# Kernel tuning notes

Hardware: AMD Instinct MI355X
Metric: run time of the kernel (lower is better)

## Reference

```python
import jax, jax.numpy as jnp
import numpy as np

B, N, C = 128, 2048, 3
VL, PN = 256, 128  # vector_length, prediction_num
NEG_SLOPE = 0.01   # torch LeakyReLU default
BN_EPS = 1e-5


def _lin(key, fin, fout):
    k1, k2 = jax.random.split(key)
    lim = 1.0 / np.sqrt(fin)
    W = jax.random.uniform(k1, (fin, fout), minval=-lim, maxval=lim, dtype=jnp.float32)
    b = jax.random.uniform(k2, (fout,), minval=-lim, maxval=lim, dtype=jnp.float32)
    return W, b


def setup_inputs() -> dict:
    key = jax.random.key(0)
    ks = jax.random.split(key, 14)
    x = jax.random.normal(ks[0], (B, N, C), dtype=jnp.float32)
    lengths = jnp.maximum(jax.random.randint(ks[1], (B,), 0, N), 1).astype(jnp.int32)
    eps = jax.random.normal(ks[2], (B, VL), dtype=jnp.float32)
    W1, b1 = _lin(ks[3], C, 64)
    W2, b2 = _lin(ks[4], 64, 64)
    W3, b3 = _lin(ks[5], 64, 128)
    W4, b4 = _lin(ks[6], 128, 1024)
    Wf, bf = _lin(ks[7], 1024, 1024)
    Wmu, bmu = _lin(ks[8], 1024, VL)
    Wlv, blv = _lin(ks[9], 1024, VL)
    Wd1, bd1 = _lin(ks[10], VL, 1024)
    Wd2, bd2 = _lin(ks[11], 1024, 1024)
    Wd3, bd3 = _lin(ks[12], 1024, PN * C)
    g1 = jnp.ones((1024,), jnp.float32); be1 = jnp.zeros((1024,), jnp.float32)
    g2 = jnp.ones((1024,), jnp.float32); be2 = jnp.zeros((1024,), jnp.float32)
    return dict(x=x, lengths=lengths, eps=eps,
                W1=W1, b1=b1, W2=W2, b2=b2, W3=W3, b3=b3, W4=W4, b4=b4,
                Wf=Wf, bf=bf, Wmu=Wmu, bmu=bmu, Wlv=Wlv, blv=blv,
                Wd1=Wd1, bd1=bd1, g1=g1, be1=be1,
                Wd2=Wd2, bd2=bd2, g2=g2, be2=be2,
                Wd3=Wd3, bd3=bd3)


def _lrelu(h):
    return jnp.where(h > 0, h, NEG_SLOPE * h)


def _bn(h, g, b):
    # BatchNorm1d in training mode: biased batch stats
    m = h.mean(axis=0)
    v = h.var(axis=0)
    return (h - m) * jax.lax.rsqrt(v + BN_EPS) * g + b


def reference(x, lengths, eps,
              W1, b1, W2, b2, W3, b3, W4, b4,
              Wf, bf, Wmu, bmu, Wlv, blv,
              Wd1, bd1, g1, be1, Wd2, bd2, g2, be2, Wd3, bd3):
    # --- pointnet per-point MLP (batched over padded [B,N,C]) ---
    h = _lrelu(x @ W1 + b1)          # [B,N,64]
    h = _lrelu(h @ W2 + b2)          # [B,N,64]
    h = _lrelu(h @ W3 + b3)          # [B,N,128]
    h = _lrelu(h @ W4 + b4)          # [B,N,1024]
    # masked max over points (ragged -> padded+mask)
    mask = jnp.arange(N)[None, :] < lengths[:, None]   # [B,N]
    h = jnp.where(mask[:, :, None], h, -jnp.inf)
    pooled = jnp.max(h, axis=1)      # [B,1024]
    # --- encoder head ---
    e = _lrelu(pooled @ Wf + bf)
    mu = e @ Wmu + bmu               # [B,VL]
    logvar = e @ Wlv + blv           # [B,VL]
    # --- reparameterize ---
    z = mu + eps * jnp.exp(0.5 * logvar)
    # --- decoder: Linear+BN+LeakyReLU x2, final Linear ---
    d = _lrelu(_bn(z @ Wd1 + bd1, g1, be1))
    d = _lrelu(_bn(d @ Wd2 + bd2, g2, be2))
    y = (d @ Wd3 + bd3).reshape(-1, PN, C)   # [B,PN,C]
    return (y, mu, logvar)
```

## Files before the change

kernel.cpp:

```cpp
#include <hip/hip_runtime.h>
#include <hip/hip_bf16.h>
#include <math.h>

#define NEG_SLOPE 0.01f

typedef short short8 __attribute__((ext_vector_type(8)));
typedef float f32x4 __attribute__((ext_vector_type(4)));

__device__ __forceinline__ float lrelu(float v) { return v > 0.0f ? v : NEG_SLOPE * v; }

__device__ __forceinline__ short f2bf(float f) {
    __hip_bfloat16 h = __float2bfloat16(f);
    return __builtin_bit_cast(short, h);
}
__device__ __forceinline__ float bf2f(short s) {
    __hip_bfloat16 h = __builtin_bit_cast(__hip_bfloat16, s);
    return __bfloat162float(h);
}

__global__ __launch_bounds__(256) void pack_all(
    const float* __restrict__ W4, const float* __restrict__ Wf,
    const float* __restrict__ Wmu, const float* __restrict__ Wlv,
    const float* __restrict__ Wd1, const float* __restrict__ Wd2,
    const float* __restrict__ Wd3, const float* __restrict__ W2,
    const float* __restrict__ W3,
    short* __restrict__ F4, short* __restrict__ Ff, short* __restrict__ Fmuvl,
    short* __restrict__ Fd1, short* __restrict__ Fd2, short* __restrict__ Fd3,
    short* __restrict__ F2, short* __restrict__ F3)
{
    int bid = blockIdx.x;
    const float* src = nullptr; short* dst = nullptr; int K = 0, N = 0; int muvl = 0;
    if      (bid < 64)   { src = W4;  dst = F4;    K = 128;  N = 1024; }
    else if (bid < 576)  { src = Wf;  dst = Ff;    K = 1024; N = 1024; bid -= 64; }
    else if (bid < 832)  { src = nullptr; dst = Fmuvl; K = 1024; N = 512; muvl = 1; bid -= 576; }
    else if (bid < 960)  { src = Wd1; dst = Fd1;   K = 256;  N = 1024; bid -= 832; }
    else if (bid < 1472) { src = Wd2; dst = Fd2;   K = 1024; N = 1024; bid -= 960; }
    else if (bid < 1664) { src = Wd3; dst = Fd3;   K = 1024; N = 384;  bid -= 1472; }
    else if (bid < 1666) { src = W2;  dst = F2;    K = 64;   N = 64;   bid -= 1664; }
    else                 { src = W3;  dst = F3;    K = 64;   N = 128;  bid -= 1666; }

    const int fragid = bid * 4 + (threadIdx.x >> 6);
    const int lane   = threadIdx.x & 63;
    const int K32    = K >> 5;
    const int t   = fragid / (K32 * 4);
    const int rem = fragid - t * K32 * 4;
    const int ks  = rem >> 2;
    const int n   = rem & 3;
    const int col   = t * 64 + n * 16 + (lane & 15);
    const int kbase = ks * 32 + (lane >> 4) * 8;

    short8 v;
#pragma unroll
    for (int e = 0; e < 8; ++e) {
        float f;
        if (muvl) f = (col < 256) ? Wmu[(size_t)(kbase + e) * 256 + col]
                                  : Wlv[(size_t)(kbase + e) * 256 + col - 256];
        else      f = src[(size_t)(kbase + e) * N + col];
        v[e] = f2bf(f);
    }
    *(short8*)&dst[(size_t)fragid * 512 + lane * 8] = v;
}

#define LOADPAIR(BUF, T, P)                                                   \
    _Pragma("unroll")                                                         \
    for (int kk = 0; kk < 2; ++kk)                                            \
        _Pragma("unroll")                                                     \
        for (int n = 0; n < 4; ++n)                                           \
            BUF[kk * 4 + n] = *(const short8*)&F4[                            \
                (size_t)(((((T) * 4 + (P) * 2 + kk) * 4) + n) * 64 + lane) * 8];

#define MFMAPAIR(BUF, KS0)                                                    \
    _Pragma("unroll")                                                         \
    for (int kk = 0; kk < 2; ++kk)                                            \
        _Pragma("unroll")                                                     \
        for (int n = 0; n < 4; ++n)                                           \
            _Pragma("unroll")                                                 \
            for (int m = 0; m < 4; ++m)                                       \
                acc[m][n] = __builtin_amdgcn_mfma_f32_16x16x32_bf16(          \
                    af[m][(KS0) + kk], BUF[kk * 4 + n], acc[m][n], 0, 0, 0);

__global__ __launch_bounds__(128, 2) void fused_pointnet_kernel(
    const float* __restrict__ x, const int* __restrict__ lengths,
    const float* __restrict__ W1, const float* __restrict__ b1,
    const float* __restrict__ b2, const float* __restrict__ b3,
    const short* __restrict__ F2, const short* __restrict__ F3,
    const short* __restrict__ F4,
    short* __restrict__ partials)
{
    const int tid   = threadIdx.x;
    const int b     = blockIdx.x & 127;
    const int chunk = blockIdx.x >> 7;
    const int len   = lengths[b];
    if (chunk * 128 >= len) return;

    __shared__ short At[128 * 128];
    const int lane = tid & 63;
    const int w    = tid >> 6;
    short* Aw = At + w * 8192;
    const int gid  = b * 2048 + chunk * 128 + tid;

    {
        const float x0 = x[gid * 3 + 0];
        const float x1 = x[gid * 3 + 1];
        const float x2 = x[gid * 3 + 2];
#pragma unroll
        for (int q = 0; q < 8; ++q) {
            short8 pv;
#pragma unroll
            for (int e = 0; e < 8; ++e) {
                int c = q * 8 + e;
                float v = b1[c];
                v = fmaf(x0, W1[c], v);
                v = fmaf(x1, W1[64 + c], v);
                v = fmaf(x2, W1[128 + c], v);
                pv[e] = f2bf(lrelu(v));
            }
            *(short8*)&Aw[lane * 64 + ((q ^ (lane & 7)) * 8)] = pv;
        }
    }

    {
        short8 a2[4][2];
#pragma unroll
        for (int m = 0; m < 4; ++m)
#pragma unroll
            for (int ks = 0; ks < 2; ++ks) {
                int rl = m * 16 + (lane & 15);
                int kch = ks * 4 + (lane >> 4);
                a2[m][ks] = *(const short8*)&Aw[rl * 64 + ((kch ^ (rl & 7)) * 8)];
            }
        short8 b2f[2][4];
#pragma unroll
        for (int ks = 0; ks < 2; ++ks)
#pragma unroll
            for (int n = 0; n < 4; ++n)
                b2f[ks][n] = *(const short8*)&F2[(size_t)(ks * 4 + n) * 512 + lane * 8];

        f32x4 acc2[4][4];
#pragma unroll
        for (int m = 0; m < 4; ++m)
#pragma unroll
            for (int n = 0; n < 4; ++n) acc2[m][n] = 0;
#pragma unroll
        for (int ks = 0; ks < 2; ++ks)
#pragma unroll
            for (int n = 0; n < 4; ++n)
#pragma unroll
                for (int m = 0; m < 4; ++m)
                    acc2[m][n] = __builtin_amdgcn_mfma_f32_16x16x32_bf16(
                        a2[m][ks], b2f[ks][n], acc2[m][n], 0, 0, 0);

#pragma unroll
        for (int n = 0; n < 4; ++n) {
            int col = n * 16 + (lane & 15);
            float bv = b2[col];
            int colch = col >> 3;
#pragma unroll
            for (int m = 0; m < 4; ++m)
#pragma unroll
                for (int r = 0; r < 4; ++r) {
                    int rl = m * 16 + (lane >> 4) * 4 + r;
                    Aw[4096 + rl * 64 + ((colch ^ (rl & 7)) * 8) + (col & 7)] =
                        f2bf(lrelu(acc2[m][n][r] + bv));
                }
        }
    }

    short8 a3[4][2];
#pragma unroll
    for (int m = 0; m < 4; ++m)
#pragma unroll
        for (int ks = 0; ks < 2; ++ks) {
            int rl = m * 16 + (lane & 15);
            int kch = ks * 4 + (lane >> 4);
            a3[m][ks] = *(const short8*)&Aw[4096 + rl * 64 + ((kch ^ (rl & 7)) * 8)];
        }
#pragma unroll
    for (int half = 0; half < 2; ++half) {
        short8 b3f[2][4];
#pragma unroll
        for (int ks = 0; ks < 2; ++ks)
#pragma unroll
            for (int n = 0; n < 4; ++n)
                b3f[ks][n] = *(const short8*)&F3[(size_t)(half * 8 + ks * 4 + n) * 512 + lane * 8];

        f32x4 acc3[4][4];
#pragma unroll
        for (int m = 0; m < 4; ++m)
#pragma unroll
            for (int n = 0; n < 4; ++n) acc3[m][n] = 0;
#pragma unroll
        for (int ks = 0; ks < 2; ++ks)
#pragma unroll
            for (int n = 0; n < 4; ++n)
#pragma unroll
                for (int m = 0; m < 4; ++m)
                    acc3[m][n] = __builtin_amdgcn_mfma_f32_16x16x32_bf16(
                        a3[m][ks], b3f[ks][n], acc3[m][n], 0, 0, 0);

#pragma unroll
        for (int n = 0; n < 4; ++n) {
            int col = half * 64 + n * 16 + (lane & 15);
            float bv = b3[col];
            int colch = col >> 3;
#pragma unroll
            for (int m = 0; m < 4; ++m)
#pragma unroll
                for (int r = 0; r < 4; ++r) {
                    int rl = m * 16 + (lane >> 4) * 4 + r;
                    Aw[rl * 128 + ((colch ^ (rl & 7)) * 8) + (col & 7)] =
                        f2bf(lrelu(acc3[m][n][r] + bv));
                }
        }
    }

    short8 af[4][4];
#pragma unroll
    for (int m = 0; m < 4; ++m)
#pragma unroll
        for (int ks = 0; ks < 4; ++ks) {
            int rl = m * 16 + (lane & 15);
            int ch = (ks * 4 + (lane >> 4)) ^ (rl & 7);
            af[m][ks] = *(const short8*)&Aw[rl * 128 + ch * 8];
        }

    const size_t pb = ((size_t)(b * 16 + chunk) * 2 + w) * 1024;

    short8 bufA[8], bufB[8];
    LOADPAIR(bufA, 0, 0);
    for (int t = 0; t < 16; ++t) {
        f32x4 acc[4][4];
#pragma unroll
        for (int m = 0; m < 4; ++m)
#pragma unroll
            for (int n = 0; n < 4; ++n) acc[m][n] = 0;

        LOADPAIR(bufB, t, 1);
        MFMAPAIR(bufA, 0);
        if (t < 15) LOADPAIR(bufA, t + 1, 0);
        MFMAPAIR(bufB, 2);

#pragma unroll
        for (int n = 0; n < 4; ++n) {
            float v = -INFINITY;
#pragma unroll
            for (int m = 0; m < 4; ++m)
#pragma unroll
                for (int r = 0; r < 4; ++r) {
                    int rloc = w * 64 + m * 16 + (lane >> 4) * 4 + r;
                    bool valid = (chunk * 128 + rloc) < len;
                    v = fmaxf(v, valid ? acc[m][n][r] : -INFINITY);
                }
            v = fmaxf(v, __shfl_xor(v, 16));
            v = fmaxf(v, __shfl_xor(v, 32));
            if (lane < 16) partials[pb + t * 64 + n * 16 + lane] = f2bf(v);
        }
    }
}

__global__ __launch_bounds__(256) void reduce_pool_kernel(
    const short* __restrict__ partials, const int* __restrict__ lengths,
    const float* __restrict__ b4, short* __restrict__ pooled)
{
    const int b = blockIdx.x;
    const int nlive = (lengths[b] + 127) >> 7;
    for (int i = threadIdx.x; i < 1024; i += 256) {
        float m = -INFINITY;
        for (int j = 0; j < nlive; ++j) {
            m = fmaxf(m, bf2f(partials[((size_t)(b * 16 + j) * 2 + 0) * 1024 + i]));
            m = fmaxf(m, bf2f(partials[((size_t)(b * 16 + j) * 2 + 1) * 1024 + i]));
        }
        pooled[(size_t)b * 1024 + i] = f2bf(lrelu(m + b4[i]));
    }
}

template<int MF>
__global__ __launch_bounds__(256) void gemm_tail(
    const short* __restrict__ A, const short* __restrict__ Wfrag,
    const float* __restrict__ bias,
    const float* __restrict__ g, const float* __restrict__ be,
    float* __restrict__ outF, short* __restrict__ outB,
    int K, int Nout, int flags)
{
    __shared__ float bns[4][32];
    __shared__ float bnq[4][32];

    const int tid = threadIdx.x, lane = tid & 63, w = tid >> 6;
    const int K32 = K >> 5;
    const int c0  = blockIdx.x * 32;
    const int tt  = blockIdx.x >> 1;
    const int hf  = blockIdx.x & 1;
    const int row0  = (MF == 2) ? 0 : blockIdx.y * 64;
    const int arow0 = row0 + w * (MF * 16) + (lane & 15);
    const int koff  = (lane >> 4) * 8;

    f32x4 acc[MF][2];
#pragma unroll
    for (int m = 0; m < MF; ++m) { acc[m][0] = 0; acc[m][1] = 0; }

    short8 aC[MF], bC[2], aN[MF], bN[2];
#pragma unroll
    for (int m = 0; m < MF; ++m)
        aC[m] = *(const short8*)&A[(size_t)(arow0 + m * 16) * K + koff];
#pragma unroll
    for (int n = 0; n < 2; ++n)
        bC[n] = *(const short8*)&Wfrag[(size_t)((tt * K32) * 4 + hf * 2 + n) * 512 + lane * 8];

    for (int ks = 0; ks < K32; ks += 2) {
#pragma unroll
        for (int m = 0; m < MF; ++m)
            aN[m] = *(const short8*)&A[(size_t)(arow0 + m * 16) * K + (ks + 1) * 32 + koff];
#pragma unroll
        for (int n = 0; n < 2; ++n)
            bN[n] = *(const short8*)&Wfrag[(size_t)((tt * K32 + ks + 1) * 4 + hf * 2 + n) * 512 + lane * 8];
#pragma unroll
        for (int n = 0; n < 2; ++n)
#pragma unroll
            for (int m = 0; m < MF; ++m)
                acc[m][n] = __builtin_amdgcn_mfma_f32_16x16x32_bf16(aC[m], bC[n], acc[m][n], 0, 0, 0);
        if (ks + 2 < K32) {
#pragma unroll
            for (int m = 0; m < MF; ++m)
                aC[m] = *(const short8*)&A[(size_t)(arow0 + m * 16) * K + (ks + 2) * 32 + koff];
#pragma unroll
            for (int n = 0; n < 2; ++n)
                bC[n] = *(const short8*)&Wfrag[(size_t)((tt * K32 + ks + 2) * 4 + hf * 2 + n) * 512 + lane * 8];
        }
#pragma unroll
        for (int n = 0; n < 2; ++n)
#pragma unroll
            for (int m = 0; m < MF; ++m)
                acc[m][n] = __builtin_amdgcn_mfma_f32_16x16x32_bf16(aN[m], bN[n], acc[m][n], 0, 0, 0);
    }

    if ((flags & 2) && MF == 2) {
#pragma unroll
        for (int n = 0; n < 2; ++n) {
            float s = 0.f, q = 0.f;
#pragma unroll
            for (int m = 0; m < MF; ++m)
#pragma unroll
                for (int r = 0; r < 4; ++r) {
                    float v = acc[m][n][r];
                    s += v; q = fmaf(v, v, q);
                }
            s += __shfl_xor(s, 16); s += __shfl_xor(s, 32);
            q += __shfl_xor(q, 16); q += __shfl_xor(q, 32);
            if (lane < 16) { bns[w][n * 16 + lane] = s; bnq[w][n * 16 + lane] = q; }
        }
        __syncthreads();
#pragma unroll
        for (int n = 0; n < 2; ++n) {
            int cl = n * 16 + (lane & 15);
            float s = bns[0][cl] + bns[1][cl] + bns[2][cl] + bns[3][cl];
            float q = bnq[0][cl] + bnq[1][cl] + bnq[2][cl] + bnq[3][cl];
            float mean = s * (1.0f / 128.0f);
            float var  = q * (1.0f / 128.0f) - mean * mean;
            float rs   = 1.0f / sqrtf(var + 1e-5f);
            float gg   = g[c0 + cl] * rs;
            float bb   = be[c0 + cl] - mean * gg;
#pragma unroll
            for (int m = 0; m < MF; ++m)
#pragma unroll
                for (int r = 0; r < 4; ++r)
                    acc[m][n][r] = fmaf(acc[m][n][r], gg, bb);
        }
    } else if (bias) {
#pragma unroll
        for (int n = 0; n < 2; ++n) {
            float bv = bias[c0 + n * 16 + (lane & 15)];
#pragma unroll
            for (int m = 0; m < MF; ++m)
#pragma unroll
                for (int r = 0; r < 4; ++r) acc[m][n][r] += bv;
        }
    }

    if (flags & 1) {
#pragma unroll
        for (int m = 0; m < MF; ++m)
#pragma unroll
            for (int n = 0; n < 2; ++n)
#pragma unroll
                for (int r = 0; r < 4; ++r) acc[m][n][r] = lrelu(acc[m][n][r]);
    }

#pragma unroll
    for (int m = 0; m < MF; ++m)
#pragma unroll
        for (int n = 0; n < 2; ++n)
#pragma unroll
            for (int r = 0; r < 4; ++r) {
                int row = row0 + w * (MF * 16) + m * 16 + (lane >> 4) * 4 + r;
                int col = c0 + n * 16 + (lane & 15);
                if (flags & 4) outB[(size_t)row * Nout + col] = f2bf(acc[m][n][r]);
                else           outF[(size_t)row * Nout + col] = acc[m][n][r];
            }
}

__global__ __launch_bounds__(256) void gemm_muvlz(
    const short* __restrict__ A, const short* __restrict__ Fmuvl,
    const float* __restrict__ bmu, const float* __restrict__ blv,
    const float* __restrict__ eps,
    float* __restrict__ mu_out, float* __restrict__ lv_out,
    short* __restrict__ zbuf)
{
    const int tid = threadIdx.x, lane = tid & 63, w = tid >> 6;
    const int c0 = blockIdx.x * 32;
    const int tt = blockIdx.x >> 1;
    const int hf = blockIdx.x & 1;
    const int row0 = blockIdx.y * 64;
    const int arow = row0 + w * 16 + (lane & 15);
    const int koff = (lane >> 4) * 8;

    f32x4 macc[2], lacc[2];
#pragma unroll
    for (int n = 0; n < 2; ++n) { macc[n] = 0; lacc[n] = 0; }

    short8 aC, bmC[2], blC[2], aN, bmN[2], blN[2];
    aC = *(const short8*)&A[(size_t)arow * 1024 + koff];
#pragma unroll
    for (int n = 0; n < 2; ++n) {
        bmC[n] = *(const short8*)&Fmuvl[(size_t)((tt * 32) * 4 + hf * 2 + n) * 512 + lane * 8];
        blC[n] = *(const short8*)&Fmuvl[(size_t)(((tt + 4) * 32) * 4 + hf * 2 + n) * 512 + lane * 8];
    }

    for (int ks = 0; ks < 32; ks += 2) {
        aN = *(const short8*)&A[(size_t)arow * 1024 + (ks + 1) * 32 + koff];
#pragma unroll
        for (int n = 0; n < 2; ++n) {
            bmN[n] = *(const short8*)&Fmuvl[(size_t)((tt * 32 + ks + 1) * 4 + hf * 2 + n) * 512 + lane * 8];
            blN[n] = *(const short8*)&Fmuvl[(size_t)(((tt + 4) * 32 + ks + 1) * 4 + hf * 2 + n) * 512 + lane * 8];
        }
#pragma unroll
        for (int n = 0; n < 2; ++n) {
            macc[n] = __builtin_amdgcn_mfma_f32_16x16x32_bf16(aC, bmC[n], macc[n], 0, 0, 0);
            lacc[n] = __builtin_amdgcn_mfma_f32_16x16x32_bf16(aC, blC[n], lacc[n], 0, 0, 0);
        }
        if (ks + 2 < 32) {
            aC = *(const short8*)&A[(size_t)arow * 1024 + (ks + 2) * 32 + koff];
#pragma unroll
            for (int n = 0; n < 2; ++n) {
                bmC[n] = *(const short8*)&Fmuvl[(size_t)((tt * 32 + ks + 2) * 4 + hf * 2 + n) * 512 + lane * 8];
                blC[n] = *(const short8*)&Fmuvl[(size_t)(((tt + 4) * 32 + ks + 2) * 4 + hf * 2 + n) * 512 + lane * 8];
            }
        }
#pragma unroll
        for (int n = 0; n < 2; ++n) {
            macc[n] = __builtin_amdgcn_mfma_f32_16x16x32_bf16(aN, bmN[n], macc[n], 0, 0, 0);
            lacc[n] = __builtin_amdgcn_mfma_f32_16x16x32_bf16(aN, blN[n], lacc[n], 0, 0, 0);
        }
    }

#pragma unroll
    for (int n = 0; n < 2; ++n) {
        int col = c0 + n * 16 + (lane & 15);
        float bmv = bmu[col], blvv = blv[col];
#pragma unroll
        for (int r = 0; r < 4; ++r) {
            int row = row0 + w * 16 + (lane >> 4) * 4 + r;
            float mu = macc[n][r] + bmv;
            float lv = lacc[n][r] + blvv;
            mu_out[(size_t)row * 256 + col] = mu;
            lv_out[(size_t)row * 256 + col] = lv;
            float z = fmaf(eps[(size_t)row * 256 + col], expf(0.5f * lv), mu);
            zbuf[(size_t)row * 256 + col] = f2bf(z);
        }
    }
}

extern "C" void kernel_launch(void* const* d_in, const int* in_sizes, int n_in,
                              void* d_out, int out_size, void* d_ws, size_t ws_size,
                              hipStream_t stream)
{
    const float* x       = (const float*)d_in[0];
    const int*   lengths = (const int*)  d_in[1];
    const float* eps     = (const float*)d_in[2];
    const float* W1  = (const float*)d_in[3];  const float* b1  = (const float*)d_in[4];
    const float* W2  = (const float*)d_in[5];  const float* b2  = (const float*)d_in[6];
    const float* W3  = (const float*)d_in[7];  const float* b3  = (const float*)d_in[8];
    const float* W4  = (const float*)d_in[9];  const float* b4  = (const float*)d_in[10];
    const float* Wf  = (const float*)d_in[11]; const float* bf  = (const float*)d_in[12];
    const float* Wmu = (const float*)d_in[13]; const float* bmu = (const float*)d_in[14];
    const float* Wlv = (const float*)d_in[15]; const float* blv = (const float*)d_in[16];
    const float* Wd1 = (const float*)d_in[17];
    const float* g1  = (const float*)d_in[19]; const float* be1 = (const float*)d_in[20];
    const float* Wd2 = (const float*)d_in[21];
    const float* g2  = (const float*)d_in[23]; const float* be2 = (const float*)d_in[24];
    const float* Wd3 = (const float*)d_in[25]; const float* bd3 = (const float*)d_in[26];

    float* out = (float*)d_out;
    float* y_out  = out;
    float* mu_out = out + 49152;
    float* lv_out = out + 81920;

    char* ws = (char*)d_ws;
    short* F4    = (short*)(ws + 0);
    short* Ff    = (short*)(ws + 262144);
    short* Fmuvl = (short*)(ws + 2359296);
    short* Fd1   = (short*)(ws + 3407872);
    short* Fd2   = (short*)(ws + 3932160);
    short* Fd3   = (short*)(ws + 6029312);
    short* F2    = (short*)(ws + 6815744);
    short* F3    = (short*)(ws + 6823936);
    short* partials = (short*)(ws + 6840320);
    short* pooled = (short*)(ws + 15228928);
    short* ebuf   = (short*)(ws + 15491072);
    short* zbuf   = (short*)(ws + 15753216);
    short* d1v    = (short*)(ws + 15818752);
    short* d2v    = (short*)(ws + 16080896);

    pack_all<<<1670, 256, 0, stream>>>(W4, Wf, Wmu, Wlv, Wd1, Wd2, Wd3, W2, W3,
                                       F4, Ff, Fmuvl, Fd1, Fd2, Fd3, F2, F3);
    fused_pointnet_kernel<<<2048, 128, 0, stream>>>(
        x, lengths, W1, b1, b2, b3, F2, F3, F4, partials);
    reduce_pool_kernel<<<128, 256, 0, stream>>>(partials, lengths, b4, pooled);
    gemm_tail<1><<<dim3(32, 2), 256, 0, stream>>>(pooled, Ff, bf, nullptr, nullptr,
                                                  nullptr, ebuf, 1024, 1024, 1 | 4);
    gemm_muvlz<<<dim3(8, 2), 256, 0, stream>>>(ebuf, Fmuvl, bmu, blv, eps,
                                               mu_out, lv_out, zbuf);
    gemm_tail<2><<<32, 256, 0, stream>>>(zbuf, Fd1, nullptr, g1, be1,
                                         nullptr, d1v, 256, 1024, 1 | 2 | 4);
    gemm_tail<2><<<32, 256, 0, stream>>>(d1v, Fd2, nullptr, g2, be2,
                                         nullptr, d2v, 1024, 1024, 1 | 2 | 4);
    gemm_tail<1><<<dim3(12, 2), 256, 0, stream>>>(d2v, Fd3, bd3, nullptr, nullptr,
                                                  y_out, nullptr, 1024, 384, 0);
}
```

Before: 147.8 us.

## Stage W4 fragments in shared memory across four waves of 256-point blocks

The pointnet kernel now uses 256-thread blocks covering 256 points each, so four waves share W4 fragment tiles. The tiles are double-buffered in LDS via register staging and __syncthreads, instead of each wave streaming all of W4 from global memory. Masking is precomputed and skipped entirely for full chunks, and the reduction kernel is adjusted to the new partial layout. The tail GEMMs turn K into a template parameter with fully unrolled loops in place of manual software pipelining. The change adds LDS traffic and a barrier per tile, and the larger blocks may reduce occupancy.

```diff
diff --git a/kernel.cpp b/kernel.cpp
--- a/kernel.cpp
+++ b/kernel.cpp
@@ -61,25 +61,7 @@
     *(short8*)&dst[(size_t)fragid * 512 + lane * 8] = v;
 }
 
-#define LOADPAIR(BUF, T, P)                                                   \
-    _Pragma("unroll")                                                         \
-    for (int kk = 0; kk < 2; ++kk)                                            \
-        _Pragma("unroll")                                                     \
-        for (int n = 0; n < 4; ++n)                                           \
-            BUF[kk * 4 + n] = *(const short8*)&F4[                            \
-                (size_t)(((((T) * 4 + (P) * 2 + kk) * 4) + n) * 64 + lane) * 8];
-
-#define MFMAPAIR(BUF, KS0)                                                    \
-    _Pragma("unroll")                                                         \
-    for (int kk = 0; kk < 2; ++kk)                                            \
-        _Pragma("unroll")                                                     \
-        for (int n = 0; n < 4; ++n)                                           \
-            _Pragma("unroll")                                                 \
-            for (int m = 0; m < 4; ++m)                                       \
-                acc[m][n] = __builtin_amdgcn_mfma_f32_16x16x32_bf16(          \
-                    af[m][(KS0) + kk], BUF[kk * 4 + n], acc[m][n], 0, 0, 0);
-
-__global__ __launch_bounds__(128, 2) void fused_pointnet_kernel(
+__global__ __launch_bounds__(256, 2) void fused_pointnet_kernel(
     const float* __restrict__ x, const int* __restrict__ lengths,
     const float* __restrict__ W1, const float* __restrict__ b1,
     const float* __restrict__ b2, const float* __restrict__ b3,
@@ -87,17 +69,17 @@
     const short* __restrict__ F4,
     short* __restrict__ partials)
 {
-    const int tid   = threadIdx.x;
-    const int b     = blockIdx.x & 127;
-    const int chunk = blockIdx.x >> 7;
-    const int len   = lengths[b];
-    if (chunk * 128 >= len) return;
-
-    __shared__ short At[128 * 128];
+    const int tid = threadIdx.x;
+    const int b   = blockIdx.x & 127;
+    const int sc  = blockIdx.x >> 7;
+    const int len = lengths[b];
+    if (sc * 256 >= len) return;
+
+    __shared__ short S[32768];
     const int lane = tid & 63;
     const int w    = tid >> 6;
-    short* Aw = At + w * 8192;
-    const int gid  = b * 2048 + chunk * 128 + tid;
+    short* Aw = S + w * 8192;
+    const int gid = b * 2048 + sc * 256 + tid;
 
     {
         const float x0 = x[gid * 3 + 0];
@@ -166,51 +148,53 @@
         }
     }
 
-    short8 a3[4][2];
-#pragma unroll
-    for (int m = 0; m < 4; ++m)
-#pragma unroll
-        for (int ks = 0; ks < 2; ++ks) {
-            int rl = m * 16 + (lane & 15);
-            int kch = ks * 4 + (lane >> 4);
-            a3[m][ks] = *(const short8*)&Aw[4096 + rl * 64 + ((kch ^ (rl & 7)) * 8)];
-        }
-#pragma unroll
-    for (int half = 0; half < 2; ++half) {
-        short8 b3f[2][4];
-#pragma unroll
-        for (int ks = 0; ks < 2; ++ks)
-#pragma unroll
-            for (int n = 0; n < 4; ++n)
-                b3f[ks][n] = *(const short8*)&F3[(size_t)(half * 8 + ks * 4 + n) * 512 + lane * 8];
-
-        f32x4 acc3[4][4];
+    {
+        short8 a3[4][2];
 #pragma unroll
         for (int m = 0; m < 4; ++m)
 #pragma unroll
-            for (int n = 0; n < 4; ++n) acc3[m][n] = 0;
-#pragma unroll
-        for (int ks = 0; ks < 2; ++ks)
-#pragma unroll
-            for (int n = 0; n < 4; ++n)
+            for (int ks = 0; ks < 2; ++ks) {
+                int rl = m * 16 + (lane & 15);
+                int kch = ks * 4 + (lane >> 4);
+                a3[m][ks] = *(const short8*)&Aw[4096 + rl * 64 + ((kch ^ (rl & 7)) * 8)];
+            }
+#pragma unroll
+        for (int half = 0; half < 2; ++half) {
+            short8 b3f[2][4];
+#pragma unroll
+            for (int ks = 0; ks < 2; ++ks)
+#pragma unroll
+                for (int n = 0; n < 4; ++n)
+                    b3f[ks][n] = *(const short8*)&F3[(size_t)(half * 8 + ks * 4 + n) * 512 + lane * 8];
+
+            f32x4 acc3[4][4];
+#pragma unroll
+            for (int m = 0; m < 4; ++m)
+#pragma unroll
+                for (int n = 0; n < 4; ++n) acc3[m][n] = 0;
+#pragma unroll
+            for (int ks = 0; ks < 2; ++ks)
+#pragma unroll
+                for (int n = 0; n < 4; ++n)
+#pragma unroll
+                    for (int m = 0; m < 4; ++m)
+                        acc3[m][n] = __builtin_amdgcn_mfma_f32_16x16x32_bf16(
+                            a3[m][ks], b3f[ks][n], acc3[m][n], 0, 0, 0);
+
+#pragma unroll
+            for (int n = 0; n < 4; ++n) {
+                int col = half * 64 + n * 16 + (lane & 15);
+                float bv = b3[col];
+                int colch = col >> 3;
 #pragma unroll
                 for (int m = 0; m < 4; ++m)
-                    acc3[m][n] = __builtin_amdgcn_mfma_f32_16x16x32_bf16(
-                        a3[m][ks], b3f[ks][n], acc3[m][n], 0, 0, 0);
-
-#pragma unroll
-        for (int n = 0; n < 4; ++n) {
-            int col = half * 64 + n * 16 + (lane & 15);
-            float bv = b3[col];
-            int colch = col >> 3;
-#pragma unroll
-            for (int m = 0; m < 4; ++m)
-#pragma unroll
-                for (int r = 0; r < 4; ++r) {
-                    int rl = m * 16 + (lane >> 4) * 4 + r;
-                    Aw[rl * 128 + ((colch ^ (rl & 7)) * 8) + (col & 7)] =
-                        f2bf(lrelu(acc3[m][n][r] + bv));
-                }
+#pragma unroll
+                    for (int r = 0; r < 4; ++r) {
+                        int rl = m * 16 + (lane >> 4) * 4 + r;
+                        Aw[rl * 128 + ((colch ^ (rl & 7)) * 8) + (col & 7)] =
+                            f2bf(lrelu(acc3[m][n][r] + bv));
+                    }
+            }
         }
     }
 
@@ -224,36 +208,86 @@
             af[m][ks] = *(const short8*)&Aw[rl * 128 + ch * 8];
         }
 
-    const size_t pb = ((size_t)(b * 16 + chunk) * 2 + w) * 1024;
-
-    short8 bufA[8], bufB[8];
-    LOADPAIR(bufA, 0, 0);
+    const bool full = (sc * 256 + 256) <= len;
+    float madd[4][4];
+    if (!full) {
+#pragma unroll
+        for (int m = 0; m < 4; ++m)
+#pragma unroll
+            for (int r = 0; r < 4; ++r) {
+                int rloc = sc * 256 + w * 64 + m * 16 + (lane >> 4) * 4 + r;
+                madd[m][r] = (rloc < len) ? 0.0f : -INFINITY;
+            }
+    }
+
+    short8 stg[4];
+#pragma unroll
+    for (int i = 0; i < 4; ++i)
+        stg[i] = *(const short8*)&F4[w * 2048 + i * 512 + lane * 8];
+
+    __syncthreads();
+#pragma unroll
+    for (int i = 0; i < 4; ++i)
+        *(short8*)&S[w * 2048 + i * 512 + lane * 8] = stg[i];
+
     for (int t = 0; t < 16; ++t) {
+        __syncthreads();
+        if (t < 15) {
+#pragma unroll
+            for (int i = 0; i < 4; ++i)
+                stg[i] = *(const short8*)&F4[(size_t)(t + 1) * 8192 + w * 2048 + i * 512 + lane * 8];
+        }
+
+        const short* Bb = S + (t & 1) * 8192;
         f32x4 acc[4][4];
 #pragma unroll
         for (int m = 0; m < 4; ++m)
 #pragma unroll
             for (int n = 0; n < 4; ++n) acc[m][n] = 0;
 
-        LOADPAIR(bufB, t, 1);
-        MFMAPAIR(bufA, 0);
-        if (t < 15) LOADPAIR(bufA, t + 1, 0);
-        MFMAPAIR(bufB, 2);
-
+#pragma unroll
+        for (int ks = 0; ks < 4; ++ks) {
+            short8 bfr[4];
+#pragma unroll
+            for (int n = 0; n < 4; ++n)
+                bfr[n] = *(const short8*)&Bb[(ks * 4 + n) * 512 + lane * 8];
+#pragma unroll
+            for (int n = 0; n < 4; ++n)
+#pragma unroll
+                for (int m = 0; m < 4; ++m)
+                    acc[m][n] = __builtin_amdgcn_mfma_f32_16x16x32_bf16(
+                        af[m][ks], bfr[n], acc[m][n], 0, 0, 0);
+        }
+
+        const size_t pb = ((size_t)((b * 8 + sc) * 4 + w)) * 1024 + t * 64;
 #pragma unroll
         for (int n = 0; n < 4; ++n) {
-            float v = -INFINITY;
-#pragma unroll
-            for (int m = 0; m < 4; ++m)
-#pragma unroll
-                for (int r = 0; r < 4; ++r) {
-                    int rloc = w * 64 + m * 16 + (lane >> 4) * 4 + r;
-                    bool valid = (chunk * 128 + rloc) < len;
-                    v = fmaxf(v, valid ? acc[m][n][r] : -INFINITY);
-                }
+            float v;
+            if (full) {
+                v = acc[0][n][0];
+#pragma unroll
+                for (int m = 0; m < 4; ++m)
+#pragma unroll
+                    for (int r = 0; r < 4; ++r)
+                        if (m | r) v = fmaxf(v, acc[m][n][r]);
+            } else {
+                v = -INFINITY;
+#pragma unroll
+                for (int m = 0; m < 4; ++m)
+#pragma unroll
+                    for (int r = 0; r < 4; ++r)
+                        v = fmaxf(v, acc[m][n][r] + madd[m][r]);
+            }
             v = fmaxf(v, __shfl_xor(v, 16));
             v = fmaxf(v, __shfl_xor(v, 32));
-            if (lane < 16) partials[pb + t * 64 + n * 16 + lane] = f2bf(v);
+            if (lane < 16) partials[pb + n * 16 + lane] = f2bf(v);
+        }
+
+        if (t < 15) {
+            short* Bn = S + ((t + 1) & 1) * 8192;
+#pragma unroll
+            for (int i = 0; i < 4; ++i)
+                *(short8*)&Bn[w * 2048 + i * 512 + lane * 8] = stg[i];
         }
     }
 }
@@ -263,30 +297,31 @@
     const float* __restrict__ b4, short* __restrict__ pooled)
 {
     const int b = blockIdx.x;
-    const int nlive = (lengths[b] + 127) >> 7;
+    const int nlive = (lengths[b] + 255) >> 8;
     for (int i = threadIdx.x; i < 1024; i += 256) {
         float m = -INFINITY;
         for (int j = 0; j < nlive; ++j) {
-            m = fmaxf(m, bf2f(partials[((size_t)(b * 16 + j) * 2 + 0) * 1024 + i]));
-            m = fmaxf(m, bf2f(partials[((size_t)(b * 16 + j) * 2 + 1) * 1024 + i]));
+#pragma unroll
+            for (int w = 0; w < 4; ++w)
+                m = fmaxf(m, bf2f(partials[((size_t)((b * 8 + j) * 4 + w)) * 1024 + i]));
         }
         pooled[(size_t)b * 1024 + i] = f2bf(lrelu(m + b4[i]));
     }
 }
 
-template<int MF>
+template<int MF, int K32>
 __global__ __launch_bounds__(256) void gemm_tail(
     const short* __restrict__ A, const short* __restrict__ Wfrag,
     const float* __restrict__ bias,
     const float* __restrict__ g, const float* __restrict__ be,
     float* __restrict__ outF, short* __restrict__ outB,
-    int K, int Nout, int flags)
+    int Nout, int flags)
 {
     __shared__ float bns[4][32];
     __shared__ float bnq[4][32];
 
     const int tid = threadIdx.x, lane = tid & 63, w = tid >> 6;
-    const int K32 = K >> 5;
+    const int K   = K32 * 32;
     const int c0  = blockIdx.x * 32;
     const int tt  = blockIdx.x >> 1;
     const int hf  = blockIdx.x & 1;
@@ -298,39 +333,20 @@
 #pragma unroll
     for (int m = 0; m < MF; ++m) { acc[m][0] = 0; acc[m][1] = 0; }
 
-    short8 aC[MF], bC[2], aN[MF], bN[2];
-#pragma unroll
-    for (int m = 0; m < MF; ++m)
-        aC[m] = *(const short8*)&A[(size_t)(arow0 + m * 16) * K + koff];
-#pragma unroll
-    for (int n = 0; n < 2; ++n)
-        bC[n] = *(const short8*)&Wfrag[(size_t)((tt * K32) * 4 + hf * 2 + n) * 512 + lane * 8];
-
-    for (int ks = 0; ks < K32; ks += 2) {
+#pragma unroll
+    for (int ks = 0; ks < K32; ++ks) {
+        short8 a[MF], bfr[2];
 #pragma unroll
         for (int m = 0; m < MF; ++m)
-            aN[m] = *(const short8*)&A[(size_t)(arow0 + m * 16) * K + (ks + 1) * 32 + koff];
+            a[m] = *(const short8*)&A[(size_t)(arow0 + m * 16) * K + ks * 32 + koff];
 #pragma unroll
         for (int n = 0; n < 2; ++n)
-            bN[n] = *(const short8*)&Wfrag[(size_t)((tt * K32 + ks + 1) * 4 + hf * 2 + n) * 512 + lane * 8];
+            bfr[n] = *(const short8*)&Wfrag[(size_t)((tt * K32 + ks) * 4 + hf * 2 + n) * 512 + lane * 8];
 #pragma unroll
         for (int n = 0; n < 2; ++n)
 #pragma unroll
             for (int m = 0; m < MF; ++m)
-                acc[m][n] = __builtin_amdgcn_mfma_f32_16x16x32_bf16(aC[m], bC[n], acc[m][n], 0, 0, 0);
-        if (ks + 2 < K32) {
-#pragma unroll
-            for (int m = 0; m < MF; ++m)
-                aC[m] = *(const short8*)&A[(size_t)(arow0 + m * 16) * K + (ks + 2) * 32 + koff];
-#pragma unroll
-            for (int n = 0; n < 2; ++n)
-                bC[n] = *(const short8*)&Wfrag[(size_t)((tt * K32 + ks + 2) * 4 + hf * 2 + n) * 512 + lane * 8];
-        }
-#pragma unroll
-        for (int n = 0; n < 2; ++n)
-#pragma unroll
-            for (int m = 0; m < MF; ++m)
-                acc[m][n] = __builtin_amdgcn_mfma_f32_16x16x32_bf16(aN[m], bN[n], acc[m][n], 0, 0, 0);
+                acc[m][n] = __builtin_amdgcn_mfma_f32_16x16x32_bf16(a[m], bfr[n], acc[m][n], 0, 0, 0);
     }
 
     if ((flags & 2) && MF == 2) {
@@ -417,38 +433,15 @@
 #pragma unroll
     for (int n = 0; n < 2; ++n) { macc[n] = 0; lacc[n] = 0; }
 
-    short8 aC, bmC[2], blC[2], aN, bmN[2], blN[2];
-    aC = *(const short8*)&A[(size_t)arow * 1024 + koff];
-#pragma unroll
-    for (int n = 0; n < 2; ++n) {
-        bmC[n] = *(const short8*)&Fmuvl[(size_t)((tt * 32) * 4 + hf * 2 + n) * 512 + lane * 8];
-        blC[n] = *(const short8*)&Fmuvl[(size_t)(((tt + 4) * 32) * 4 + hf * 2 + n) * 512 + lane * 8];
-    }
-
-    for (int ks = 0; ks < 32; ks += 2) {
-        aN = *(const short8*)&A[(size_t)arow * 1024 + (ks + 1) * 32 + koff];
+#pragma unroll
+    for (int ks = 0; ks < 32; ++ks) {
+        short8 a = *(const short8*)&A[(size_t)arow * 1024 + ks * 32 + koff];
 #pragma unroll
         for (int n = 0; n < 2; ++n) {
-            bmN[n] = *(const short8*)&Fmuvl[(size_t)((tt * 32 + ks + 1) * 4 + hf * 2 + n) * 512 + lane * 8];
-            blN[n] = *(const short8*)&Fmuvl[(size_t)(((tt + 4) * 32 + ks + 1) * 4 + hf * 2 + n) * 512 + lane * 8];
-        }
-#pragma unroll
-        for (int n = 0; n < 2; ++n) {
-            macc[n] = __builtin_amdgcn_mfma_f32_16x16x32_bf16(aC, bmC[n], macc[n], 0, 0, 0);
-            lacc[n] = __builtin_amdgcn_mfma_f32_16x16x32_bf16(aC, blC[n], lacc[n], 0, 0, 0);
-        }
-        if (ks + 2 < 32) {
-            aC = *(const short8*)&A[(size_t)arow * 1024 + (ks + 2) * 32 + koff];
-#pragma unroll
-            for (int n = 0; n < 2; ++n) {
-                bmC[n] = *(const short8*)&Fmuvl[(size_t)((tt * 32 + ks + 2) * 4 + hf * 2 + n) * 512 + lane * 8];
-                blC[n] = *(const short8*)&Fmuvl[(size_t)(((tt + 4) * 32 + ks + 2) * 4 + hf * 2 + n) * 512 + lane * 8];
-            }
-        }
-#pragma unroll
-        for (int n = 0; n < 2; ++n) {
-            macc[n] = __builtin_amdgcn_mfma_f32_16x16x32_bf16(aN, bmN[n], macc[n], 0, 0, 0);
-            lacc[n] = __builtin_amdgcn_mfma_f32_16x16x32_bf16(aN, blN[n], lacc[n], 0, 0, 0);
+            short8 bm = *(const short8*)&Fmuvl[(size_t)((tt * 32 + ks) * 4 + hf * 2 + n) * 512 + lane * 8];
+            short8 bl = *(const short8*)&Fmuvl[(size_t)(((tt + 4) * 32 + ks) * 4 + hf * 2 + n) * 512 + lane * 8];
+            macc[n] = __builtin_amdgcn_mfma_f32_16x16x32_bf16(a, bm, macc[n], 0, 0, 0);
+            lacc[n] = __builtin_amdgcn_mfma_f32_16x16x32_bf16(a, bl, lacc[n], 0, 0, 0);
         }
     }
 
@@ -512,17 +505,17 @@
 
     pack_all<<<1670, 256, 0, stream>>>(W4, Wf, Wmu, Wlv, Wd1, Wd2, Wd3, W2, W3,
                                        F4, Ff, Fmuvl, Fd1, Fd2, Fd3, F2, F3);
-    fused_pointnet_kernel<<<2048, 128, 0, stream>>>(
+    fused_pointnet_kernel<<<1024, 256, 0, stream>>>(
         x, lengths, W1, b1, b2, b3, F2, F3, F4, partials);
     reduce_pool_kernel<<<128, 256, 0, stream>>>(partials, lengths, b4, pooled);
-    gemm_tail<1><<<dim3(32, 2), 256, 0, stream>>>(pooled, Ff, bf, nullptr, nullptr,
-                                                  nullptr, ebuf, 1024, 1024, 1 | 4);
+    gemm_tail<1, 32><<<dim3(32, 2), 256, 0, stream>>>(pooled, Ff, bf, nullptr, nullptr,
+                                                      nullptr, ebuf, 1024, 1 | 4);
     gemm_muvlz<<<dim3(8, 2), 256, 0, stream>>>(ebuf, Fmuvl, bmu, blv, eps,
                                                mu_out, lv_out, zbuf);
-    gemm_tail<2><<<32, 256, 0, stream>>>(zbuf, Fd1, nullptr, g1, be1,
-                                         nullptr, d1v, 256, 1024, 1 | 2 | 4);
-    gemm_tail<2><<<32, 256, 0, stream>>>(d1v, Fd2, nullptr, g2, be2,
-                                         nullptr, d2v, 1024, 1024, 1 | 2 | 4);
-    gemm_tail<1><<<dim3(12, 2), 256, 0, stream>>>(d2v, Fd3, bd3, nullptr, nullptr,
-                                                  y_out, nullptr, 1024, 384, 0);
-}
+    gemm_tail<2, 8><<<32, 256, 0, stream>>>(zbuf, Fd1, nullptr, g1, be1,
+                                            nullptr, d1v, 1024, 1 | 2 | 4);
+    gemm_tail<2, 32><<<32, 256, 0, stream>>>(d1v, Fd2, nullptr, g2, be2,
+                                             nullptr, d2v, 1024, 1 | 2 | 4);
+    gemm_tail<1, 32><<<dim3(12, 2), 256, 0, stream>>>(d2v, Fd3, bd3, nullptr, nullptr,
+                                                      y_out, nullptr, 384, 0);
+}
```

Result: faster. 144.2 us (-2.4%).
